# Kernel tuning notes

Measured on AMD Instinct MI355X. Metric: run time of the kernel, lower is better.

The kernel has to match this reference:

```python
import jax, jax.numpy as jnp
import numpy as np

B, D, H, Wd = 256, 15, 63, 126  # batch, depth, lat, lon
K = 5                            # kernel == stride (reduce_resolution)
PD, PH, PW = 0, 1, 2             # ZeroPadding3D sizes
OD, OH, OW = (D + 2 * PD) // K, (H + 2 * PH) // K, (Wd + 2 * PW) // K  # 3,13,26


def setup_inputs() -> dict:
    key = jax.random.key(0)
    k1, k2, k3, k4 = jax.random.split(key, 4)
    x = jax.random.normal(k1, (B, D, H, Wd, 1), dtype=jnp.float32)
    # binary ocean mask: 1 = ocean (kept), 0 = land (removed)
    land = (jax.random.uniform(k2, (D, H, Wd, 1)) > 0.25).astype(jnp.float32)
    # positive cell volumes
    volumes = jax.random.uniform(k3, (D, H, Wd, 1), dtype=jnp.float32) + 0.5
    # per-location (non-shared) locally-connected weights
    W = jax.random.normal(k4, (OD, OH, OW, K, K, K, 1, 1), dtype=jnp.float32) / np.sqrt(K ** 3)
    b = jnp.zeros((OD, OH, OW, 1), dtype=jnp.float32)
    return {"x": x, "land": land, "volumes": volumes, "W": W, "b": b}


def reference(x, land, volumes, W, b):
    # LandValueRemoval3D (start): zero out land cells
    h = x * land
    # ZeroPadding3D((0,1,2))
    h = jnp.pad(h, ((0, 0), (0, 0), (PH, PH), (PW, PW), (0, 0)))
    # LocallyConnected3D, kernel==stride==5: non-overlapping blocks -> blocked einsum
    # (B, OD, K, OH, K, OW, K, C)
    hb = h.reshape(B, OD, K, OH, K, OW, K, 1)
    y = jnp.einsum('bipjqkrc,ijkpqrcf->bijkf', hb, W) + b  # per-location weights
    y = jax.nn.relu(y)
    # UpSampling3D((5,5,5))
    y = jnp.repeat(jnp.repeat(jnp.repeat(y, K, axis=1), K, axis=2), K, axis=3)
    # Cropping3D((0,1,2))
    y = y[:, :, PH:-PH, PW:-PW, :]
    # LandValueRemoval3D (end)
    y = y * land
    # MassConversation3D: rescale so total mass (x * volume) is conserved per sample
    mass_in = jnp.sum(x * volumes, axis=(1, 2, 3, 4), keepdims=True)
    mass_out = jnp.sum(y * volumes, axis=(1, 2, 3, 4), keepdims=True)
    return y * (mass_in / mass_out)
```

## Files before the change

### kernel.cpp

```cpp
#include <hip/hip_runtime.h>

#define BATCH 256
#define DD 15
#define HH 63
#define WW 126
#define KK 5
#define OD 3
#define OH 13
#define OWI 26
#define SPAT (DD*HH*WW)
#define HWSZ (HH*WW)
#define ROWS (KK*KK)
#define WPAD (OWI*KK)
#define NBLK (OD*OH*OWI)
#define IJN  (OD*OH)

__global__ __launch_bounds__(256)
void conv_mass_kernel(const float* __restrict__ x,
                      const float* __restrict__ land,
                      const float* __restrict__ vols,
                      const float* __restrict__ Wt,
                      const float* __restrict__ bias,
                      float* __restrict__ y_small,
                      double* __restrict__ mass_in,
                      double* __restrict__ mass_out) {
    __shared__ float lds_x[ROWS * WPAD];
    __shared__ float lds_lv[ROWS * WPAD];
    __shared__ float red_y[OWI];
    __shared__ float red_m[4];

    const int tid = threadIdx.x;
    const int bij = blockIdx.x;
    const int b  = bij / IJN;
    const int ij = bij - b * IJN;
    const int i  = ij / OH;
    const int j  = ij - i * OH;

    const float* xb = x + (size_t)b * SPAT;

    float massp = 0.f;
    const int NPAIR = ROWS * (WPAD / 2);
    for (int t = tid; t < NPAIR; t += 256) {
        int row = t / 65;
        int wp  = (t - row * 65) * 2;
        int p = row / KK, q = row - p * KK;
        int h = j * KK + q - 1;
        int w0 = wp - 2;
        float2 xl = make_float2(0.f, 0.f);
        float2 lv2 = make_float2(0.f, 0.f);
        if ((unsigned)h < (unsigned)HH && (unsigned)w0 < (unsigned)WW) {
            int d = i * KK + p;
            int sidx = (d * HH + h) * WW + w0;
            float2 xv = *reinterpret_cast<const float2*>(xb + sidx);
            float2 lv = *reinterpret_cast<const float2*>(land + sidx);
            float2 vv = *reinterpret_cast<const float2*>(vols + sidx);
            xl.x  = xv.x * lv.x;  xl.y  = xv.y * lv.y;
            lv2.x = lv.x * vv.x;  lv2.y = lv.y * vv.y;
            massp += xv.x * vv.x + xv.y * vv.y;
        }
        *reinterpret_cast<float2*>(&lds_x [row * WPAD + wp]) = xl;
        *reinterpret_cast<float2*>(&lds_lv[row * WPAD + wp]) = lv2;
    }

    #pragma unroll
    for (int s = 32; s; s >>= 1) massp += __shfl_down(massp, s, 64);
    if ((tid & 63) == 0) red_m[tid >> 6] = massp;
    __syncthreads();

    const int k    = tid >> 3;
    const int lane = tid & 7;
    if (k < OWI) {
        const float* Ws = Wt + ((size_t)ij * OWI + k) * 125;
        const int base_w = k * KK;
        float acc = 0.f, accl = 0.f;
        for (int m = lane; m < 125; m += 8) {
            int p   = m / 25;
            int rem = m - p * 25;
            int q   = rem / 5;
            int r   = rem - q * 5;
            int li  = (p * KK + q) * WPAD + base_w + r;
            acc  = fmaf(lds_x[li], Ws[m], acc);
            accl += lds_lv[li];
        }
        #pragma unroll
        for (int s = 4; s; s >>= 1) {
            acc  += __shfl_down(acc,  s, 8);
            accl += __shfl_down(accl, s, 8);
        }
        if (lane == 0) {
            float yv = fmaxf(acc + bias[ij * OWI + k], 0.f);
            y_small[(size_t)b * NBLK + ij * OWI + k] = yv;
            red_y[k] = yv * accl;
        }
    }
    __syncthreads();

    if (tid == 0) {
        float mo = 0.f;
        #pragma unroll
        for (int kk = 0; kk < OWI; ++kk) mo += red_y[kk];
        float mi = red_m[0] + red_m[1] + red_m[2] + red_m[3];
        atomicAdd(mass_out + b, (double)mo);
        atomicAdd(mass_in  + b, (double)mi);
    }
}

__global__ __launch_bounds__(256)
void out_kernel(const float* __restrict__ y_small,
                const float* __restrict__ land,
                const double* __restrict__ mass_in,
                const double* __restrict__ mass_out,
                float* __restrict__ out) {
    __shared__ float ylds[OH * OWI];
    __shared__ float s_scale;

    const int bd = blockIdx.x;
    const int b  = bd / DD;
    const int d  = bd - b * DD;
    const int i  = d / KK;
    const int tid = threadIdx.x;

    if (tid == 0) s_scale = (float)(mass_in[b] / mass_out[b]);
    __syncthreads();
    for (int t = tid; t < OH * OWI; t += 256) {
        ylds[t] = y_small[(size_t)b * NBLK + i * (OH * OWI) + t] * s_scale;
    }
    __syncthreads();

    const int lane = tid & 63;
    const int wv   = tid >> 6;
    if (lane < 63) {
        const int w0  = lane * 2;
        const int kb0 = (w0 + 2) / KK;
        const int kb1 = (w0 + 3) / KK;
        const float* landp = land + d * HWSZ + w0;
        float*       outp  = out + (size_t)b * SPAT + d * HWSZ + w0;
        for (int h = wv; h < HH; h += 4) {
            const int jb = ((h + 1) / KK) * OWI;
            float2 l2 = *reinterpret_cast<const float2*>(landp + h * WW);
            float2 o2;
            o2.x = ylds[jb + kb0] * l2.x;
            o2.y = ylds[jb + kb1] * l2.y;
            *reinterpret_cast<float2*>(outp + h * WW) = o2;
        }
    }
}

extern "C" void kernel_launch(void* const* d_in, const int* in_sizes, int n_in,
                              void* d_out, int out_size, void* d_ws, size_t ws_size,
                              hipStream_t stream) {
    const float* x    = (const float*)d_in[0];
    const float* land = (const float*)d_in[1];
    const float* vols = (const float*)d_in[2];
    const float* Wt   = (const float*)d_in[3];
    const float* bias = (const float*)d_in[4];

    char* ws = (char*)d_ws;
    double* mass_in  = (double*)(ws);
    double* mass_out = (double*)(ws + 2048);
    float*  y_small  = (float*) (ws + 4096);

    hipMemsetAsync(ws, 0, 4096, stream);

    conv_mass_kernel<<<BATCH * IJN, 256, 0, stream>>>(
        x, land, vols, Wt, bias, y_small, mass_in, mass_out);

    out_kernel<<<BATCH * DD, 256, 0, stream>>>(
        y_small, land, mass_in, mass_out, (float*)d_out);
}
```

Measured before the change: 293.6 us.

## Prefold land mask into weights and restructure conv and output kernels

Adds a prep kernel that multiplies the land mask into the locally-connected weights (padded to stride 8) and precomputes the per-block land*volume sums. The conv kernel then uses one thread per output block, reading x directly from global memory with no LDS staging. The mass ratio is applied to y_small by a separate scale kernel. The output kernel becomes a flat float4 streaming writer over pairs of samples. Weight prep is recomputed every call and adds launches; per-thread strided x reads may coalesce poorly.

```diff
diff --git a/kernel.cpp b/kernel.cpp
--- a/kernel.cpp
+++ b/kernel.cpp
@@ -4,145 +4,168 @@
 #define DD 15
 #define HH 63
 #define WW 126
-#define KK 5
 #define OD 3
 #define OH 13
 #define OWI 26
 #define SPAT (DD*HH*WW)
 #define HWSZ (HH*WW)
-#define ROWS (KK*KK)
-#define WPAD (OWI*KK)
 #define NBLK (OD*OH*OWI)
-#define IJN  (OD*OH)
+#define WSTRIDE 200
 
 __global__ __launch_bounds__(256)
-void conv_mass_kernel(const float* __restrict__ x,
-                      const float* __restrict__ land,
-                      const float* __restrict__ vols,
-                      const float* __restrict__ Wt,
-                      const float* __restrict__ bias,
-                      float* __restrict__ y_small,
-                      double* __restrict__ mass_in,
-                      double* __restrict__ mass_out) {
-    __shared__ float lds_x[ROWS * WPAD];
-    __shared__ float lds_lv[ROWS * WPAD];
-    __shared__ float red_y[OWI];
-    __shared__ float red_m[4];
-
-    const int tid = threadIdx.x;
-    const int bij = blockIdx.x;
-    const int b  = bij / IJN;
-    const int ij = bij - b * IJN;
-    const int i  = ij / OH;
-    const int j  = ij - i * OH;
-
-    const float* xb = x + (size_t)b * SPAT;
-
-    float massp = 0.f;
-    const int NPAIR = ROWS * (WPAD / 2);
-    for (int t = tid; t < NPAIR; t += 256) {
-        int row = t / 65;
-        int wp  = (t - row * 65) * 2;
-        int p = row / KK, q = row - p * KK;
-        int h = j * KK + q - 1;
-        int w0 = wp - 2;
-        float2 xl = make_float2(0.f, 0.f);
-        float2 lv2 = make_float2(0.f, 0.f);
-        if ((unsigned)h < (unsigned)HH && (unsigned)w0 < (unsigned)WW) {
-            int d = i * KK + p;
-            int sidx = (d * HH + h) * WW + w0;
-            float2 xv = *reinterpret_cast<const float2*>(xb + sidx);
-            float2 lv = *reinterpret_cast<const float2*>(land + sidx);
-            float2 vv = *reinterpret_cast<const float2*>(vols + sidx);
-            xl.x  = xv.x * lv.x;  xl.y  = xv.y * lv.y;
-            lv2.x = lv.x * vv.x;  lv2.y = lv.y * vv.y;
-            massp += xv.x * vv.x + xv.y * vv.y;
+void prep_kernel(const float* __restrict__ W, const float* __restrict__ land,
+                 const float* __restrict__ vols,
+                 float* __restrict__ Wp, float* __restrict__ lv) {
+    int idx = blockIdx.x * 256 + threadIdx.x;
+    if (idx < NBLK * WSTRIDE) {
+        int blk = idx / WSTRIDE;
+        int t   = idx - blk * WSTRIDE;
+        int row = t >> 3, e = t & 7;
+        int ij = blk / OWI, k = blk - ij * OWI;
+        int i  = ij / OH,   j = ij - i * OH;
+        int p  = row / 5,   q = row - p * 5;
+        float val = 0.f;
+        if (e < 5) {
+            int d = i * 5 + p, h = j * 5 + q - 1, w = k * 5 + e - 2;
+            if ((unsigned)h < (unsigned)HH && (unsigned)w < (unsigned)WW) {
+                val = W[blk * 125 + row * 5 + e] * land[(d * HH + h) * WW + w];
+            }
         }
-        *reinterpret_cast<float2*>(&lds_x [row * WPAD + wp]) = xl;
-        *reinterpret_cast<float2*>(&lds_lv[row * WPAD + wp]) = lv2;
-    }
-
-    #pragma unroll
-    for (int s = 32; s; s >>= 1) massp += __shfl_down(massp, s, 64);
-    if ((tid & 63) == 0) red_m[tid >> 6] = massp;
-    __syncthreads();
-
-    const int k    = tid >> 3;
-    const int lane = tid & 7;
-    if (k < OWI) {
-        const float* Ws = Wt + ((size_t)ij * OWI + k) * 125;
-        const int base_w = k * KK;
-        float acc = 0.f, accl = 0.f;
-        for (int m = lane; m < 125; m += 8) {
-            int p   = m / 25;
-            int rem = m - p * 25;
-            int q   = rem / 5;
-            int r   = rem - q * 5;
-            int li  = (p * KK + q) * WPAD + base_w + r;
-            acc  = fmaf(lds_x[li], Ws[m], acc);
-            accl += lds_lv[li];
+        Wp[idx] = val;
+    } else if (idx < NBLK * WSTRIDE + NBLK) {
+        int blk = idx - NBLK * WSTRIDE;
+        int ij = blk / OWI, k = blk - ij * OWI;
+        int i  = ij / OH,   j = ij - i * OH;
+        float s = 0.f;
+        for (int p = 0; p < 5; ++p) {
+            int d = i * 5 + p;
+            for (int q = 0; q < 5; ++q) {
+                int h = j * 5 + q - 1;
+                if ((unsigned)h >= (unsigned)HH) continue;
+                int base = (d * HH + h) * WW;
+                for (int r = 0; r < 5; ++r) {
+                    int w = k * 5 + r - 2;
+                    if ((unsigned)w < (unsigned)WW)
+                        s += land[base + w] * vols[base + w];
+                }
+            }
         }
-        #pragma unroll
-        for (int s = 4; s; s >>= 1) {
-            acc  += __shfl_down(acc,  s, 8);
-            accl += __shfl_down(accl, s, 8);
-        }
-        if (lane == 0) {
-            float yv = fmaxf(acc + bias[ij * OWI + k], 0.f);
-            y_small[(size_t)b * NBLK + ij * OWI + k] = yv;
-            red_y[k] = yv * accl;
-        }
-    }
-    __syncthreads();
-
-    if (tid == 0) {
-        float mo = 0.f;
-        #pragma unroll
-        for (int kk = 0; kk < OWI; ++kk) mo += red_y[kk];
-        float mi = red_m[0] + red_m[1] + red_m[2] + red_m[3];
-        atomicAdd(mass_out + b, (double)mo);
-        atomicAdd(mass_in  + b, (double)mi);
+        lv[blk] = s;
     }
 }
 
 __global__ __launch_bounds__(256)
-void out_kernel(const float* __restrict__ y_small,
-                const float* __restrict__ land,
-                const double* __restrict__ mass_in,
-                const double* __restrict__ mass_out,
-                float* __restrict__ out) {
-    __shared__ float ylds[OH * OWI];
-    __shared__ float s_scale;
+void conv_kernel(const float* __restrict__ x, const float* __restrict__ vols,
+                 const float* __restrict__ Wp, const float* __restrict__ lv,
+                 const float* __restrict__ bias,
+                 float* __restrict__ y_small,
+                 double* __restrict__ mass_in, double* __restrict__ mass_out) {
+    __shared__ float redf[8];
+    const int tid = threadIdx.x;
+    const int b   = blockIdx.x >> 2;
+    const int blk = ((blockIdx.x & 3) << 8) + tid;
+    const bool live = blk < NBLK;
 
-    const int bd = blockIdx.x;
-    const int b  = bd / DD;
-    const int d  = bd - b * DD;
-    const int i  = d / KK;
-    const int tid = threadIdx.x;
+    const float* xb = x + (size_t)b * SPAT;
 
-    if (tid == 0) s_scale = (float)(mass_in[b] / mass_out[b]);
-    __syncthreads();
-    for (int t = tid; t < OH * OWI; t += 256) {
-        ylds[t] = y_small[(size_t)b * NBLK + i * (OH * OWI) + t] * s_scale;
+    float acc = 0.f;
+    float mi  = 0.f;
+    float mo  = 0.f;
+
+    if (live) {
+        int ij = blk / OWI, k = blk - ij * OWI;
+        int i  = ij / OH,   j = ij - i * OH;
+        const int h0 = j * 5 - 1;
+        const int w0 = k * 5 - 2;
+        const float* wp = Wp + blk * WSTRIDE;
+        for (int p = 0; p < 5; ++p) {
+            const int d = i * 5 + p;
+            #pragma unroll
+            for (int q = 0; q < 5; ++q) {
+                const int h = h0 + q;
+                if ((unsigned)h < (unsigned)HH) {
+                    const int base = (d * HH + h) * WW + w0;
+                    const float* wr = wp + (p * 5 + q) * 8;
+                    const float4 w4 = *reinterpret_cast<const float4*>(wr);
+                    const float  w4e = wr[4];
+                    #pragma unroll
+                    for (int r = 0; r < 5; ++r) {
+                        const int w = w0 + r;
+                        if ((unsigned)w < (unsigned)WW) {
+                            const float xv = xb[base + r];
+                            const float wv = (r == 0) ? w4.x : (r == 1) ? w4.y
+                                           : (r == 2) ? w4.z : (r == 3) ? w4.w : w4e;
+                            acc = fmaf(xv, wv, acc);
+                            mi  = fmaf(xv, vols[base + r], mi);
+                        }
+                    }
+                }
+            }
+        }
+        const float yv = fmaxf(acc + bias[blk], 0.f);
+        y_small[(size_t)b * NBLK + blk] = yv;
+        mo = yv * lv[blk];
+    }
+
+    #pragma unroll
+    for (int s = 32; s; s >>= 1) {
+        mi += __shfl_down(mi, s, 64);
+        mo += __shfl_down(mo, s, 64);
+    }
+    if ((tid & 63) == 0) {
+        redf[(tid >> 6) * 2]     = mi;
+        redf[(tid >> 6) * 2 + 1] = mo;
     }
     __syncthreads();
+    if (tid == 0) {
+        float tmi = redf[0] + redf[2] + redf[4] + redf[6];
+        float tmo = redf[1] + redf[3] + redf[5] + redf[7];
+        atomicAdd(mass_in  + b, (double)tmi);
+        atomicAdd(mass_out + b, (double)tmo);
+    }
+}
 
-    const int lane = tid & 63;
-    const int wv   = tid >> 6;
-    if (lane < 63) {
-        const int w0  = lane * 2;
-        const int kb0 = (w0 + 2) / KK;
-        const int kb1 = (w0 + 3) / KK;
-        const float* landp = land + d * HWSZ + w0;
-        float*       outp  = out + (size_t)b * SPAT + d * HWSZ + w0;
-        for (int h = wv; h < HH; h += 4) {
-            const int jb = ((h + 1) / KK) * OWI;
-            float2 l2 = *reinterpret_cast<const float2*>(landp + h * WW);
-            float2 o2;
-            o2.x = ylds[jb + kb0] * l2.x;
-            o2.y = ylds[jb + kb1] * l2.y;
-            *reinterpret_cast<float2*>(outp + h * WW) = o2;
+__global__ __launch_bounds__(256)
+void scale_y_kernel(const double* __restrict__ mi, const double* __restrict__ mo,
+                    float* __restrict__ y_small) {
+    __shared__ float ss;
+    const int b = blockIdx.x;
+    if (threadIdx.x == 0) ss = (float)(mi[b] / mo[b]);
+    __syncthreads();
+    for (int t = threadIdx.x; t < NBLK; t += 256)
+        y_small[(size_t)b * NBLK + t] *= ss;
+}
+
+__global__ __launch_bounds__(256)
+void out_kernel(const float* __restrict__ y, const float* __restrict__ land,
+                float4* __restrict__ out) {
+    const unsigned PAIR4 = (2u * SPAT) / 4u;
+    const unsigned CH    = 3721u;
+    const unsigned b2    = blockIdx.x >> 4;
+    const unsigned chunk = blockIdx.x & 15u;
+    const unsigned begin = chunk * CH;
+    const unsigned end   = (begin + CH < PAIR4) ? begin + CH : PAIR4;
+    const unsigned base4 = b2 * PAIR4;
+
+    for (unsigned t = begin + threadIdx.x; t < end; t += 256) {
+        const unsigned e0 = t * 4u;
+        float o[4];
+        #pragma unroll
+        for (int u = 0; u < 4; ++u) {
+            const unsigned re = e0 + u;
+            const unsigned bo = re >= (unsigned)SPAT;
+            const unsigned r  = re - (bo ? (unsigned)SPAT : 0u);
+            const unsigned d  = r / HWSZ;
+            const unsigned r2 = r - d * HWSZ;
+            const unsigned h  = r2 / WW;
+            const unsigned w  = r2 - h * WW;
+            const unsigned i  = d / 5u;
+            const unsigned jj = (h + 1u) / 5u;
+            const unsigned kb = (w + 2u) / 5u;
+            const unsigned yidx = (b2 * 2u + bo) * NBLK + (i * OH + jj) * OWI + kb;
+            o[u] = y[yidx] * land[r];
         }
+        out[base4 + t] = make_float4(o[0], o[1], o[2], o[3]);
     }
 }
 
@@ -158,13 +181,19 @@
     char* ws = (char*)d_ws;
     double* mass_in  = (double*)(ws);
     double* mass_out = (double*)(ws + 2048);
-    float*  y_small  = (float*) (ws + 4096);
+    float*  Wp       = (float*) (ws + 4096);
+    float*  lv       = (float*) (ws + 4096 + 811200);
+    float*  y_small  = (float*) (ws + 4096 + 811200 + 4096);
 
     hipMemsetAsync(ws, 0, 4096, stream);
 
-    conv_mass_kernel<<<BATCH * IJN, 256, 0, stream>>>(
-        x, land, vols, Wt, bias, y_small, mass_in, mass_out);
+    prep_kernel<<<(NBLK * WSTRIDE + NBLK + 255) / 256, 256, 0, stream>>>(
+        Wt, land, vols, Wp, lv);
 
-    out_kernel<<<BATCH * DD, 256, 0, stream>>>(
-        y_small, land, mass_in, mass_out, (float*)d_out);
+    conv_kernel<<<BATCH * 4, 256, 0, stream>>>(
+        x, vols, Wp, lv, bias, y_small, mass_in, mass_out);
+
+    scale_y_kernel<<<BATCH, 256, 0, stream>>>(mass_in, mass_out, y_small);
+
+    out_kernel<<<128 * 16, 256, 0, stream>>>(y_small, land, (float4*)d_out);
 }
```

New measurement: 377.7 us. 1.29x slower.
